# Optimization experiments

Measured on AMD Instinct MI355X. Metric: run time of the kernel, lower is better.

## Reference

```python
import jax, jax.numpy as jnp
import numpy as np

DIM = 1024
NUM_HEADS = 16
HEAD_DIM = DIM // NUM_HEADS


def setup_inputs() -> dict:
    key = jax.random.key(0)
    ks = jax.random.split(key, 9)
    s = 1.0 / np.sqrt(DIM)
    x = jax.random.normal(ks[0], (2, 2048, DIM), dtype=jnp.float32)
    Wq = jax.random.normal(ks[1], (DIM, DIM), dtype=jnp.float32) * s
    bq = jax.random.normal(ks[2], (DIM,), dtype=jnp.float32) * s
    Wk = jax.random.normal(ks[3], (DIM, DIM), dtype=jnp.float32) * s
    bk = jax.random.normal(ks[4], (DIM,), dtype=jnp.float32) * s
    Wv = jax.random.normal(ks[5], (DIM, DIM), dtype=jnp.float32) * s
    bv = jax.random.normal(ks[6], (DIM,), dtype=jnp.float32) * s
    Wo = jax.random.normal(ks[7], (DIM, DIM), dtype=jnp.float32) * s
    bo = jax.random.normal(ks[8], (DIM,), dtype=jnp.float32) * s
    return {"x": x, "Wq": Wq, "bq": bq, "Wk": Wk, "bk": bk,
            "Wv": Wv, "bv": bv, "Wo": Wo, "bo": bo}


def _softmax_one(x, axis=-1):
    # softmax with +1 in the denominator (quiet attention)
    x = x - jnp.max(x, axis=axis, keepdims=True)
    ex = jnp.exp(x)
    return ex / (1.0 + jnp.sum(ex, axis=axis, keepdims=True))


def reference(x, Wq, bq, Wk, bk, Wv, bv, Wo, bo):
    B, L, D = x.shape
    H, hd = NUM_HEADS, HEAD_DIM
    q = (x @ Wq + bq).reshape(B, L, H, hd).transpose(0, 2, 1, 3)  # b h l d
    k = (x @ Wk + bk).reshape(B, L, H, hd).transpose(0, 2, 1, 3)
    v = (x @ Wv + bv).reshape(B, L, H, hd).transpose(0, 2, 1, 3)
    scores = jnp.einsum('bhqd,bhkd->bhqk', q, k) / np.sqrt(hd).astype(np.float32)
    # causal additive mask: -inf above the diagonal (matches torch generate_square_subsequent_mask)
    causal = jnp.triu(jnp.full((L, L), -jnp.inf, dtype=scores.dtype), k=1)
    scores = scores + causal
    attn = _softmax_one(scores, axis=-1)
    ctx = jnp.einsum('bhqk,bhkd->bhqd', attn, v)
    ctx = ctx.transpose(0, 2, 1, 3).reshape(B, L, D)
    return ctx @ Wo + bo
```

## Files before the change

kernel.cpp:

```cpp
#include <hip/hip_runtime.h>
#include <hip/hip_bf16.h>
#include <cstdint>
#include <cstddef>

#define DIMN 1024
#define NHEAD 16
#define HDIM 64
#define NB 2
#define SEQ 2048
#define MROWS 4096
#define BHN 32
#define QKV_STRIDE 4194304
#define BH_ELEMS 131072

typedef float f32x4 __attribute__((ext_vector_type(4)));
typedef __bf16 bf16x8 __attribute__((ext_vector_type(8)));

__device__ __forceinline__ void async_copy16(const void* g, void* l) {
    __builtin_amdgcn_global_load_lds(
        (__attribute__((address_space(1))) void*)(g),
        (__attribute__((address_space(3))) void*)(l), 16, 0, 0);
}

__device__ __forceinline__ unsigned short bf16_bits(float f) {
    __hip_bfloat16 hb = __float2bfloat16(f);
    return *(unsigned short*)&hb;
}

__global__ __launch_bounds__(256) void prep_kernel(
        const float* __restrict__ x, const float* __restrict__ bq,
        const float* __restrict__ bk, const float* __restrict__ bv,
        __hip_bfloat16* __restrict__ xbf, float* __restrict__ biasq) {
    int bid = blockIdx.x;
    if (bid < 4096) {
        int i = (bid * 256 + threadIdx.x) * 4;
        float4 v = *(const float4*)(x + i);
        xbf[i + 0] = __float2bfloat16(v.x);
        xbf[i + 1] = __float2bfloat16(v.y);
        xbf[i + 2] = __float2bfloat16(v.z);
        xbf[i + 3] = __float2bfloat16(v.w);
    } else {
        int base = (bid - 4096) * 1024 + threadIdx.x * 4;
#pragma unroll
        for (int e = 0; e < 4; e++) {
            int gi = base + e;
            int which = gi >> 10, off = gi & 1023;
            float v = (which == 0) ? bq[off] : (which == 1) ? bk[off] : bv[off];
            biasq[gi] = v;
        }
    }
}

__global__ __launch_bounds__(256) void transpose_w_kernel(
        const float* __restrict__ Wq, const float* __restrict__ Wk,
        const float* __restrict__ Wv, const float* __restrict__ Wo,
        __hip_bfloat16* __restrict__ wqkvt, __hip_bfloat16* __restrict__ wot) {
    __shared__ float tile[32][33];
    int z = blockIdx.z;
    const float* in = (z == 0) ? Wq : (z == 1) ? Wk : (z == 2) ? Wv : Wo;
    __hip_bfloat16* out = (z == 3) ? wot : wqkvt + (size_t)z * DIMN * DIMN;
    int n0 = blockIdx.x * 32, k0 = blockIdx.y * 32;
    int tx = threadIdx.x, ty = threadIdx.y;
#pragma unroll
    for (int r = 0; r < 32; r += 8)
        tile[ty + r][tx] = in[(size_t)(k0 + ty + r) * DIMN + n0 + tx];
    __syncthreads();
#pragma unroll
    for (int r = 0; r < 32; r += 8)
        out[(size_t)(n0 + ty + r) * DIMN + k0 + tx] =
            __float2bfloat16(tile[tx][ty + r]);
}

__global__ __launch_bounds__(256) void gemm_qkv_kernel(
        const __hip_bfloat16* __restrict__ A, const __hip_bfloat16* __restrict__ Bt,
        const float* __restrict__ bias, __hip_bfloat16* __restrict__ qkv,
        __hip_bfloat16* __restrict__ vt) {
    __shared__ __align__(16) unsigned short As[128 * 32];
    __shared__ __align__(16) unsigned short Bs[128 * 32];
    const int t = threadIdx.x;
    const int m0 = blockIdx.y * 128;
    const int n0 = blockIdx.x * 128;
    const int lane = t & 63;
    const int w = t >> 6;
    const int wm = (w >> 1) * 64;
    const int wn = (w & 1) * 64;
    const int r16 = lane & 15;
    const int quad = lane >> 4;

    f32x4 acc[4][4];
#pragma unroll
    for (int i = 0; i < 4; i++)
#pragma unroll
        for (int j = 0; j < 4; j++) acc[i][j] = (f32x4){0.f, 0.f, 0.f, 0.f};

    const int rowA = t >> 2;
    const int kch = (t & 3) * 8;

    for (int k0 = 0; k0 < DIMN; k0 += 32) {
        __syncthreads();
#pragma unroll
        for (int r = 0; r < 2; r++) {
            int row = rowA + r * 64;
            async_copy16(A + (size_t)(m0 + row) * DIMN + k0 + kch,
                         (char*)As + (size_t)(row * 4 + (t & 3)) * 16);
            async_copy16(Bt + (size_t)(n0 + row) * DIMN + k0 + kch,
                         (char*)Bs + (size_t)(row * 4 + (t & 3)) * 16);
        }
        __syncthreads();

        bf16x8 af[4], bfr[4];
#pragma unroll
        for (int i = 0; i < 4; i++)
            af[i] = *(const bf16x8*)&As[(wm + i * 16 + r16) * 32 + quad * 8];
#pragma unroll
        for (int j = 0; j < 4; j++)
            bfr[j] = *(const bf16x8*)&Bs[(wn + j * 16 + r16) * 32 + quad * 8];
#pragma unroll
        for (int i = 0; i < 4; i++)
#pragma unroll
            for (int j = 0; j < 4; j++)
                acc[i][j] = __builtin_amdgcn_mfma_f32_16x16x32_bf16(
                    af[i], bfr[j], acc[i][j], 0, 0, 0);
    }

#pragma unroll
    for (int i = 0; i < 4; i++)
#pragma unroll
        for (int j = 0; j < 4; j++) {
            int n = n0 + wn + j * 16 + r16;
            float bv = bias[n];
            int which = n >> 10, rem = n & 1023;
            int h = rem >> 6, d = rem & 63;
            int mbase = m0 + wm + i * 16 + quad * 4;
            int b = mbase >> 11;
            int lrow = mbase & 2047;
            int bh = b * NHEAD + h;
            if (which == 2) {
                ushort4 pk;
                pk.x = bf16_bits(acc[i][j][0] + bv);
                pk.y = bf16_bits(acc[i][j][1] + bv);
                pk.z = bf16_bits(acc[i][j][2] + bv);
                pk.w = bf16_bits(acc[i][j][3] + bv);
                *(ushort4*)(vt + (size_t)bh * BH_ELEMS + (size_t)d * SEQ + lrow) = pk;
            } else {
#pragma unroll
                for (int r = 0; r < 4; r++) {
                    float v = acc[i][j][r] + bv;
                    if (which == 0) v *= 0.125f;
                    qkv[(size_t)which * QKV_STRIDE + (size_t)bh * BH_ELEMS +
                        (size_t)(lrow + r) * 64 + d] = __float2bfloat16(v);
                }
            }
        }
}

__global__ __launch_bounds__(256) void gemm_out_kernel(
        const __hip_bfloat16* __restrict__ A, const __hip_bfloat16* __restrict__ Bt,
        const float* __restrict__ bias, float* __restrict__ outp) {
    __shared__ __align__(16) unsigned short As[64 * 32];
    __shared__ __align__(16) unsigned short Bs[128 * 32];
    const int t = threadIdx.x;
    const int m0 = blockIdx.y * 64;
    const int n0 = blockIdx.x * 128;
    const int lane = t & 63;
    const int w = t >> 6;
    const int wm = (w >> 1) * 32;
    const int wn = (w & 1) * 64;
    const int r16 = lane & 15;
    const int quad = lane >> 4;

    f32x4 acc[2][4];
#pragma unroll
    for (int i = 0; i < 2; i++)
#pragma unroll
        for (int j = 0; j < 4; j++) acc[i][j] = (f32x4){0.f, 0.f, 0.f, 0.f};

    const int rowA = t >> 2;
    const int kch = (t & 3) * 8;

    for (int k0 = 0; k0 < DIMN; k0 += 32) {
        __syncthreads();
        async_copy16(A + (size_t)(m0 + rowA) * DIMN + k0 + kch, (char*)As + t * 16);
#pragma unroll
        for (int r = 0; r < 2; r++) {
            int row = rowA + r * 64;
            async_copy16(Bt + (size_t)(n0 + row) * DIMN + k0 + kch,
                         (char*)Bs + (size_t)(row * 4 + (t & 3)) * 16);
        }
        __syncthreads();

        bf16x8 af[2], bfr[4];
#pragma unroll
        for (int i = 0; i < 2; i++)
            af[i] = *(const bf16x8*)&As[(wm + i * 16 + r16) * 32 + quad * 8];
#pragma unroll
        for (int j = 0; j < 4; j++)
            bfr[j] = *(const bf16x8*)&Bs[(wn + j * 16 + r16) * 32 + quad * 8];
#pragma unroll
        for (int i = 0; i < 2; i++)
#pragma unroll
            for (int j = 0; j < 4; j++)
                acc[i][j] = __builtin_amdgcn_mfma_f32_16x16x32_bf16(
                    af[i], bfr[j], acc[i][j], 0, 0, 0);
    }

#pragma unroll
    for (int i = 0; i < 2; i++)
#pragma unroll
        for (int j = 0; j < 4; j++) {
            int n = n0 + wn + j * 16 + r16;
            float bv = bias[n];
#pragma unroll
            for (int r = 0; r < 4; r++) {
                int m = m0 + wm + i * 16 + quad * 4 + r;
                outp[(size_t)m * DIMN + n] = acc[i][j][r] + bv;
            }
        }
}

__global__ __launch_bounds__(512, 4) void attn_mfma_kernel(
        const __hip_bfloat16* __restrict__ qkv, const __hip_bfloat16* __restrict__ vt,
        __hip_bfloat16* __restrict__ ctxout) {
    __shared__ __align__(16) unsigned short SMEM[24576];

    const int bx = blockIdx.x;
    const int g = bx >> 5;
    const int qt = (g < 8) ? 15 - g : g - 8;
    const int bh = bx & 31;
    const int t = threadIdx.x;
    const int lane = t & 63;
    const int w = t >> 6;
    const int half = w >> 2;
    const int wq = w & 3;
    const int r16 = lane & 15;
    const int quad = lane >> 4;
    const int qbase = qt * 128 + wq * 32;
    const int swz = quad ^ ((r16 >> 1) & 3);
    const int pkey = (r16 >> 1) & 3;

    const __hip_bfloat16* Qg = qkv + (size_t)bh * BH_ELEMS;
    const __hip_bfloat16* Kg = qkv + (size_t)QKV_STRIDE + (size_t)bh * BH_ELEMS;
    const __hip_bfloat16* Vtg = vt + (size_t)bh * BH_ELEMS;

    const unsigned short* KsW = SMEM + half * 4096;
    const unsigned short* VsW = SMEM + 8192 + half * 4096;
    unsigned short* PsW = SMEM + 16384 + w * 1024;

    bf16x8 bq[2][2];
#pragma unroll
    for (int ng = 0; ng < 2; ng++)
#pragma unroll
        for (int kp = 0; kp < 2; kp++)
            bq[ng][kp] = *(const bf16x8*)(Qg + (size_t)(qbase + ng * 16 + r16) * 64 +
                                          kp * 32 + quad * 8);

    f32x4 oT[4][2];
#pragma unroll
    for (int mt = 0; mt < 4; mt++)
#pragma unroll
        for (int ng = 0; ng < 2; ng++) oT[mt][ng] = (f32x4){0.f, 0.f, 0.f, 0.f};
    float m_run[2] = {-1e30f, -1e30f};
    float z_run[2] = {0.f, 0.f};

    const int niter = qt + 1;
#pragma unroll 1
    for (int i = 0; i < niter; i++) {
        const int kt0 = i, kt1 = qt + 1 + i;
        __syncthreads();
#pragma unroll
        for (int it = 0; it < 4; it++) {
            int cl = it * 512 + t;
            int cb = cl & 511;
            int kp = cb >> 8, rr = (cb >> 2) & 63, c = cb & 3;
            int cg = c ^ ((rr >> 1) & 3);
            int ktile = ((cl >> 9) & 1) ? kt1 : kt0;
            const __hip_bfloat16* src = (cl < 1024)
                ? Kg + (size_t)(ktile * 64 + rr) * 64 + kp * 32 + cg * 8
                : Vtg + (size_t)rr * SEQ + ktile * 64 + kp * 32 + cg * 8;
            async_copy16(src, (char*)SMEM + (size_t)cl * 16);
        }
        __syncthreads();

        const int ktile = half ? kt1 : kt0;
        if (ktile * 64 > qbase + 31) continue;

        f32x4 st[4][2];
#pragma unroll
        for (int mt = 0; mt < 4; mt++)
#pragma unroll
            for (int ng = 0; ng < 2; ng++) st[mt][ng] = (f32x4){0.f, 0.f, 0.f, 0.f};
#pragma unroll
        for (int mt = 0; mt < 4; mt++)
#pragma unroll
            for (int kp = 0; kp < 2; kp++) {
                bf16x8 ak = *(const bf16x8*)&KsW[kp * 2048 + (mt * 16 + r16) * 32 + swz * 8];
                st[mt][0] = __builtin_amdgcn_mfma_f32_16x16x32_bf16(ak, bq[0][kp], st[mt][0], 0, 0, 0);
                st[mt][1] = __builtin_amdgcn_mfma_f32_16x16x32_bf16(ak, bq[1][kp], st[mt][1], 0, 0, 0);
            }

        if (ktile * 64 + 63 > qbase) {
#pragma unroll
            for (int mt = 0; mt < 4; mt++) {
                int kb = ktile * 64 + mt * 16 + quad * 4;
#pragma unroll
                for (int ng = 0; ng < 2; ng++) {
                    int q = qbase + ng * 16 + r16;
#pragma unroll
                    for (int r = 0; r < 4; r++)
                        if (kb + r > q) st[mt][ng][r] = -__builtin_inff();
                }
            }
        }

#pragma unroll
        for (int p = 0; p < 2; p++) {
#pragma unroll
            for (int ml = 0; ml < 2; ml++) {
                int mt = p * 2 + ml;
#pragma unroll
                for (int ng = 0; ng < 2; ng++) {
                    float s0 = st[mt][ng][0], s1 = st[mt][ng][1];
                    float s2 = st[mt][ng][2], s3 = st[mt][ng][3];
                    m_run[ng] = fmaxf(m_run[ng], fmaxf(fmaxf(s0, s1), fmaxf(s2, s3)));
                    float p0 = __expf(s0), p1 = __expf(s1);
                    float p2 = __expf(s2), p3 = __expf(s3);
                    z_run[ng] += (p0 + p1) + (p2 + p3);
                    ushort4 pk;
                    pk.x = bf16_bits(p0); pk.y = bf16_bits(p1);
                    pk.z = bf16_bits(p2); pk.w = bf16_bits(p3);
                    int c = (ml * 2 + (quad >> 1)) ^ pkey;
                    *(ushort4*)&PsW[(ng * 16 + r16) * 32 + c * 8 + (quad & 1) * 4] = pk;
                }
            }
            bf16x8 bp0 = *(const bf16x8*)&PsW[r16 * 32 + (quad ^ pkey) * 8];
            bf16x8 bp1 = *(const bf16x8*)&PsW[(16 + r16) * 32 + (quad ^ pkey) * 8];
#pragma unroll
            for (int mt = 0; mt < 4; mt++) {
                bf16x8 av = *(const bf16x8*)&VsW[p * 2048 + (mt * 16 + r16) * 32 + swz * 8];
                oT[mt][0] = __builtin_amdgcn_mfma_f32_16x16x32_bf16(av, bp0, oT[mt][0], 0, 0, 0);
                oT[mt][1] = __builtin_amdgcn_mfma_f32_16x16x32_bf16(av, bp1, oT[mt][1], 0, 0, 0);
            }
        }
    }

#pragma unroll
    for (int off = 16; off < 64; off <<= 1)
#pragma unroll
        for (int ng = 0; ng < 2; ng++) {
            m_run[ng] = fmaxf(m_run[ng], __shfl_xor(m_run[ng], off, 64));
            z_run[ng] += __shfl_xor(z_run[ng], off, 64);
        }

    __syncthreads();
    f32x4* CbO = (f32x4*)SMEM;
    f32x4* Ml = (f32x4*)((char*)SMEM + 32768);
    if (w >= 4) {
        int w4 = w - 4;
#pragma unroll
        for (int mt = 0; mt < 4; mt++)
#pragma unroll
            for (int ng = 0; ng < 2; ng++)
                CbO[((w4 * 8 + mt * 2 + ng) << 6) + lane] = oT[mt][ng];
        f32x4 ml;
        ml[0] = m_run[0]; ml[1] = m_run[1]; ml[2] = z_run[0]; ml[3] = z_run[1];
        Ml[(w4 << 6) + lane] = ml;
    }
    __syncthreads();
    if (w < 4) {
        f32x4 ml = Ml[(w << 6) + lane];
        float rd[2];
#pragma unroll
        for (int ng = 0; ng < 2; ng++) {
            float mtot = fmaxf(m_run[ng], ml[ng]);
            float ztot = z_run[ng] + ml[2 + ng];
            rd[ng] = 1.f / (__expf(mtot) + ztot);
        }
        const int b = bh >> 4, h = bh & 15;
#pragma unroll
        for (int mt = 0; mt < 4; mt++)
#pragma unroll
            for (int ng = 0; ng < 2; ng++) {
                f32x4 O1 = CbO[((w * 8 + mt * 2 + ng) << 6) + lane];
                int q = qbase + ng * 16 + r16;
                ushort4 pk;
                pk.x = bf16_bits((oT[mt][ng][0] + O1[0]) * rd[ng]);
                pk.y = bf16_bits((oT[mt][ng][1] + O1[1]) * rd[ng]);
                pk.z = bf16_bits((oT[mt][ng][2] + O1[2]) * rd[ng]);
                pk.w = bf16_bits((oT[mt][ng][3] + O1[3]) * rd[ng]);
                *(ushort4*)(ctxout + ((size_t)(b * SEQ + q)) * DIMN + h * 64 +
                            mt * 16 + quad * 4) = pk;
            }
    }
}


extern "C" void kernel_launch(void* const* d_in, const int* in_sizes, int n_in,
                              void* d_out, int out_size, void* d_ws, size_t ws_size,
                              hipStream_t stream) {
    const float* x  = (const float*)d_in[0];
    const float* Wq = (const float*)d_in[1];
    const float* bq = (const float*)d_in[2];
    const float* Wk = (const float*)d_in[3];
    const float* bk = (const float*)d_in[4];
    const float* Wv = (const float*)d_in[5];
    const float* bv = (const float*)d_in[6];
    const float* Wo = (const float*)d_in[7];
    const float* bo = (const float*)d_in[8];

    char* ws = (char*)d_ws;
    __hip_bfloat16* xbf   = (__hip_bfloat16*)(ws);
    __hip_bfloat16* wqkvt = (__hip_bfloat16*)(ws + (8u << 20));
    __hip_bfloat16* wot   = (__hip_bfloat16*)(ws + (14u << 20));
    float*          biasq = (float*)(ws + (16u << 20));
    __hip_bfloat16* qkv   = (__hip_bfloat16*)(ws + (16u << 20) + 65536u);
    __hip_bfloat16* vt    = (__hip_bfloat16*)(ws + (16u << 20) + 65536u + (16u << 20));
    __hip_bfloat16* ctx   = (__hip_bfloat16*)(ws + (16u << 20) + 65536u + (24u << 20));
    float* out = (float*)d_out;

    prep_kernel<<<4099, 256, 0, stream>>>(x, bq, bk, bv, xbf, biasq);
    transpose_w_kernel<<<dim3(32, 32, 4), dim3(32, 8), 0, stream>>>(Wq, Wk, Wv, Wo, wqkvt, wot);

    gemm_qkv_kernel<<<dim3(24, 32), 256, 0, stream>>>(xbf, wqkvt, biasq, qkv, vt);
    attn_mfma_kernel<<<512, 512, 0, stream>>>(qkv, vt, ctx);
    gemm_out_kernel<<<dim3(8, 64), 256, 0, stream>>>(ctx, wot, bo, out);
}
```

Baseline: 184.1 us.

## Double-buffer K tiles in attention and fuse weight transpose into prep kernel

The attention loop now prefetches the next K tile pair into a second LDS buffer while the current one is being computed, and issues the V load at the start of each iteration so it overlaps the QK^T and softmax work. The P staging buffer is halved by processing one query group at a time, with an extra barrier between the score and PV phases. Separately, the weight transpose kernel is folded into the prep kernel to remove one launch. These add LDS usage and a barrier per iteration, and the async loads may not be properly waited on before use.

Result: faster. 178.2 us (-3.2%).

```diff
diff --git a/kernel.cpp b/kernel.cpp
--- a/kernel.cpp
+++ b/kernel.cpp
@@ -30,17 +30,22 @@
 __global__ __launch_bounds__(256) void prep_kernel(
         const float* __restrict__ x, const float* __restrict__ bq,
         const float* __restrict__ bk, const float* __restrict__ bv,
-        __hip_bfloat16* __restrict__ xbf, float* __restrict__ biasq) {
-    int bid = blockIdx.x;
+        const float* __restrict__ Wq, const float* __restrict__ Wk,
+        const float* __restrict__ Wv, const float* __restrict__ Wo,
+        __hip_bfloat16* __restrict__ xbf, float* __restrict__ biasq,
+        __hip_bfloat16* __restrict__ wqkvt, __hip_bfloat16* __restrict__ wot) {
+    __shared__ float tile[32][33];
+    const int bid = blockIdx.x;
+    const int t = threadIdx.x;
     if (bid < 4096) {
-        int i = (bid * 256 + threadIdx.x) * 4;
+        int i = (bid * 256 + t) * 4;
         float4 v = *(const float4*)(x + i);
         xbf[i + 0] = __float2bfloat16(v.x);
         xbf[i + 1] = __float2bfloat16(v.y);
         xbf[i + 2] = __float2bfloat16(v.z);
         xbf[i + 3] = __float2bfloat16(v.w);
-    } else {
-        int base = (bid - 4096) * 1024 + threadIdx.x * 4;
+    } else if (bid < 4099) {
+        int base = (bid - 4096) * 1024 + t * 4;
 #pragma unroll
         for (int e = 0; e < 4; e++) {
             int gi = base + e;
@@ -48,27 +53,23 @@
             float v = (which == 0) ? bq[off] : (which == 1) ? bk[off] : bv[off];
             biasq[gi] = v;
         }
-    }
-}
-
-__global__ __launch_bounds__(256) void transpose_w_kernel(
-        const float* __restrict__ Wq, const float* __restrict__ Wk,
-        const float* __restrict__ Wv, const float* __restrict__ Wo,
-        __hip_bfloat16* __restrict__ wqkvt, __hip_bfloat16* __restrict__ wot) {
-    __shared__ float tile[32][33];
-    int z = blockIdx.z;
-    const float* in = (z == 0) ? Wq : (z == 1) ? Wk : (z == 2) ? Wv : Wo;
-    __hip_bfloat16* out = (z == 3) ? wot : wqkvt + (size_t)z * DIMN * DIMN;
-    int n0 = blockIdx.x * 32, k0 = blockIdx.y * 32;
-    int tx = threadIdx.x, ty = threadIdx.y;
-#pragma unroll
-    for (int r = 0; r < 32; r += 8)
-        tile[ty + r][tx] = in[(size_t)(k0 + ty + r) * DIMN + n0 + tx];
-    __syncthreads();
-#pragma unroll
-    for (int r = 0; r < 32; r += 8)
-        out[(size_t)(n0 + ty + r) * DIMN + k0 + tx] =
-            __float2bfloat16(tile[tx][ty + r]);
+    } else {
+        int rr = bid - 4099;
+        int z = rr >> 10;
+        int tid = rr & 1023;
+        int n0 = (tid & 31) * 32, k0 = (tid >> 5) * 32;
+        const float* in = (z == 0) ? Wq : (z == 1) ? Wk : (z == 2) ? Wv : Wo;
+        __hip_bfloat16* out = (z == 3) ? wot : wqkvt + (size_t)z * DIMN * DIMN;
+        int tx = t & 31, ty = t >> 5;
+#pragma unroll
+        for (int r = 0; r < 32; r += 8)
+            tile[ty + r][tx] = in[(size_t)(k0 + ty + r) * DIMN + n0 + tx];
+        __syncthreads();
+#pragma unroll
+        for (int r = 0; r < 32; r += 8)
+            out[(size_t)(n0 + ty + r) * DIMN + k0 + tx] =
+                __float2bfloat16(tile[tx][ty + r]);
+    }
 }
 
 __global__ __launch_bounds__(256) void gemm_qkv_kernel(
@@ -221,7 +222,7 @@
 __global__ __launch_bounds__(512, 4) void attn_mfma_kernel(
         const __hip_bfloat16* __restrict__ qkv, const __hip_bfloat16* __restrict__ vt,
         __hip_bfloat16* __restrict__ ctxout) {
-    __shared__ __align__(16) unsigned short SMEM[24576];
+    __shared__ __align__(16) unsigned short SMEM[28672];
 
     const int bx = blockIdx.x;
     const int g = bx >> 5;
@@ -242,9 +243,11 @@
     const __hip_bfloat16* Kg = qkv + (size_t)QKV_STRIDE + (size_t)bh * BH_ELEMS;
     const __hip_bfloat16* Vtg = vt + (size_t)bh * BH_ELEMS;
 
-    const unsigned short* KsW = SMEM + half * 4096;
-    const unsigned short* VsW = SMEM + 8192 + half * 4096;
-    unsigned short* PsW = SMEM + 16384 + w * 1024;
+    unsigned short* PsW = SMEM + 24576 + w * 512;
+
+    const int cb_kp = (t & 511) >> 8;
+    const int cb_rr = ((t & 511) >> 2) & 63;
+    const int cb_cg = ((t & 511) & 3) ^ ((cb_rr >> 1) & 3);
 
     bf16x8 bq[2][2];
 #pragma unroll
@@ -263,60 +266,74 @@
     float z_run[2] = {0.f, 0.f};
 
     const int niter = qt + 1;
+
+#pragma unroll
+    for (int it = 0; it < 2; it++) {
+        int cl = it * 512 + t;
+        int ktile = (cl >> 9) ? (qt + 1) : 0;
+        async_copy16(Kg + (size_t)(ktile * 64 + cb_rr) * 64 + cb_kp * 32 + cb_cg * 8,
+                     (char*)SMEM + (size_t)cl * 16);
+    }
+
 #pragma unroll 1
     for (int i = 0; i < niter; i++) {
-        const int kt0 = i, kt1 = qt + 1 + i;
-        __syncthreads();
-#pragma unroll
-        for (int it = 0; it < 4; it++) {
+        const int curb = i & 1;
+        __syncthreads();
+
+#pragma unroll
+        for (int it = 0; it < 2; it++) {
             int cl = it * 512 + t;
-            int cb = cl & 511;
-            int kp = cb >> 8, rr = (cb >> 2) & 63, c = cb & 3;
-            int cg = c ^ ((rr >> 1) & 3);
-            int ktile = ((cl >> 9) & 1) ? kt1 : kt0;
-            const __hip_bfloat16* src = (cl < 1024)
-                ? Kg + (size_t)(ktile * 64 + rr) * 64 + kp * 32 + cg * 8
-                : Vtg + (size_t)rr * SEQ + ktile * 64 + kp * 32 + cg * 8;
-            async_copy16(src, (char*)SMEM + (size_t)cl * 16);
-        }
-        __syncthreads();
-
-        const int ktile = half ? kt1 : kt0;
-        if (ktile * 64 > qbase + 31) continue;
+            int ktile = (cl >> 9) ? (qt + 1 + i) : i;
+            async_copy16(Vtg + (size_t)cb_rr * SEQ + ktile * 64 + cb_kp * 32 + cb_cg * 8,
+                         (char*)SMEM + 32768 + (size_t)cl * 16);
+        }
+        if (i + 1 < niter) {
+            int ktA = i + 1;
+            int ktB = qt + 2 + i; if (ktB > 31) ktB = 31;
+#pragma unroll
+            for (int it = 0; it < 2; it++) {
+                int cl = it * 512 + t;
+                int ktile = (cl >> 9) ? ktB : ktA;
+                async_copy16(Kg + (size_t)(ktile * 64 + cb_rr) * 64 + cb_kp * 32 + cb_cg * 8,
+                             (char*)SMEM + (size_t)(curb ^ 1) * 16384 + (size_t)cl * 16);
+            }
+        }
+
+        const int ktile = half ? (qt + 1 + i) : i;
+        const bool active = (ktile * 64 <= qbase + 31);
 
         f32x4 st[4][2];
-#pragma unroll
-        for (int mt = 0; mt < 4; mt++)
-#pragma unroll
-            for (int ng = 0; ng < 2; ng++) st[mt][ng] = (f32x4){0.f, 0.f, 0.f, 0.f};
-#pragma unroll
-        for (int mt = 0; mt < 4; mt++)
-#pragma unroll
-            for (int kp = 0; kp < 2; kp++) {
-                bf16x8 ak = *(const bf16x8*)&KsW[kp * 2048 + (mt * 16 + r16) * 32 + swz * 8];
-                st[mt][0] = __builtin_amdgcn_mfma_f32_16x16x32_bf16(ak, bq[0][kp], st[mt][0], 0, 0, 0);
-                st[mt][1] = __builtin_amdgcn_mfma_f32_16x16x32_bf16(ak, bq[1][kp], st[mt][1], 0, 0, 0);
-            }
-
-        if (ktile * 64 + 63 > qbase) {
-#pragma unroll
-            for (int mt = 0; mt < 4; mt++) {
-                int kb = ktile * 64 + mt * 16 + quad * 4;
-#pragma unroll
-                for (int ng = 0; ng < 2; ng++) {
-                    int q = qbase + ng * 16 + r16;
-#pragma unroll
-                    for (int r = 0; r < 4; r++)
-                        if (kb + r > q) st[mt][ng][r] = -__builtin_inff();
+        if (active) {
+            const unsigned short* KsW = SMEM + curb * 8192 + half * 4096;
+#pragma unroll
+            for (int mt = 0; mt < 4; mt++)
+#pragma unroll
+                for (int ng = 0; ng < 2; ng++) st[mt][ng] = (f32x4){0.f, 0.f, 0.f, 0.f};
+#pragma unroll
+            for (int mt = 0; mt < 4; mt++)
+#pragma unroll
+                for (int kp = 0; kp < 2; kp++) {
+                    bf16x8 ak = *(const bf16x8*)&KsW[kp * 2048 + (mt * 16 + r16) * 32 + swz * 8];
+                    st[mt][0] = __builtin_amdgcn_mfma_f32_16x16x32_bf16(ak, bq[0][kp], st[mt][0], 0, 0, 0);
+                    st[mt][1] = __builtin_amdgcn_mfma_f32_16x16x32_bf16(ak, bq[1][kp], st[mt][1], 0, 0, 0);
                 }
-            }
-        }
-
-#pragma unroll
-        for (int p = 0; p < 2; p++) {
-#pragma unroll
-            for (int ml = 0; ml < 2; ml++) {
-                int mt = p * 2 + ml;
+
+            if (ktile * 64 + 63 > qbase) {
+#pragma unroll
+                for (int mt = 0; mt < 4; mt++) {
+                    int kb = ktile * 64 + mt * 16 + quad * 4;
+#pragma unroll
+                    for (int ng = 0; ng < 2; ng++) {
+                        int q = qbase + ng * 16 + r16;
+#pragma unroll
+                        for (int r = 0; r < 4; r++)
+                            if (kb + r > q) st[mt][ng][r] = -__builtin_inff();
+                    }
+                }
+            }
+
+#pragma unroll
+            for (int mt = 0; mt < 4; mt++)
 #pragma unroll
                 for (int ng = 0; ng < 2; ng++) {
                     float s0 = st[mt][ng][0], s1 = st[mt][ng][1];
@@ -325,20 +342,37 @@
                     float p0 = __expf(s0), p1 = __expf(s1);
                     float p2 = __expf(s2), p3 = __expf(s3);
                     z_run[ng] += (p0 + p1) + (p2 + p3);
-                    ushort4 pk;
-                    pk.x = bf16_bits(p0); pk.y = bf16_bits(p1);
-                    pk.z = bf16_bits(p2); pk.w = bf16_bits(p3);
-                    int c = (ml * 2 + (quad >> 1)) ^ pkey;
-                    *(ushort4*)&PsW[(ng * 16 + r16) * 32 + c * 8 + (quad & 1) * 4] = pk;
+                    st[mt][ng][0] = p0; st[mt][ng][1] = p1;
+                    st[mt][ng][2] = p2; st[mt][ng][3] = p3;
                 }
-            }
-            bf16x8 bp0 = *(const bf16x8*)&PsW[r16 * 32 + (quad ^ pkey) * 8];
-            bf16x8 bp1 = *(const bf16x8*)&PsW[(16 + r16) * 32 + (quad ^ pkey) * 8];
-#pragma unroll
-            for (int mt = 0; mt < 4; mt++) {
-                bf16x8 av = *(const bf16x8*)&VsW[p * 2048 + (mt * 16 + r16) * 32 + swz * 8];
-                oT[mt][0] = __builtin_amdgcn_mfma_f32_16x16x32_bf16(av, bp0, oT[mt][0], 0, 0, 0);
-                oT[mt][1] = __builtin_amdgcn_mfma_f32_16x16x32_bf16(av, bp1, oT[mt][1], 0, 0, 0);
+        }
+        __syncthreads();
+
+        if (active) {
+            const unsigned short* VsW = SMEM + 16384 + half * 4096;
+#pragma unroll
+            for (int p = 0; p < 2; p++) {
+#pragma unroll
+                for (int ng = 0; ng < 2; ng++) {
+#pragma unroll
+                    for (int ml = 0; ml < 2; ml++) {
+                        int mt = p * 2 + ml;
+                        ushort4 pk;
+                        pk.x = bf16_bits(st[mt][ng][0]);
+                        pk.y = bf16_bits(st[mt][ng][1]);
+                        pk.z = bf16_bits(st[mt][ng][2]);
+                        pk.w = bf16_bits(st[mt][ng][3]);
+                        int c = (ml * 2 + (quad >> 1)) ^ pkey;
+                        *(ushort4*)&PsW[r16 * 32 + c * 8 + (quad & 1) * 4] = pk;
+                    }
+                    bf16x8 bp = *(const bf16x8*)&PsW[r16 * 32 + (quad ^ pkey) * 8];
+#pragma unroll
+                    for (int mt = 0; mt < 4; mt++) {
+                        bf16x8 av = *(const bf16x8*)&VsW[p * 2048 + (mt * 16 + r16) * 32 + swz * 8];
+                        oT[mt][ng] = __builtin_amdgcn_mfma_f32_16x16x32_bf16(
+                            av, bp, oT[mt][ng], 0, 0, 0);
+                    }
+                }
             }
         }
     }
@@ -417,9 +451,8 @@
     __hip_bfloat16* ctx   = (__hip_bfloat16*)(ws + (16u << 20) + 65536u + (24u << 20));
     float* out = (float*)d_out;
 
-    prep_kernel<<<4099, 256, 0, stream>>>(x, bq, bk, bv, xbf, biasq);
-    transpose_w_kernel<<<dim3(32, 32, 4), dim3(32, 8), 0, stream>>>(Wq, Wk, Wv, Wo, wqkvt, wot);
-
+    prep_kernel<<<8195, 256, 0, stream>>>(x, bq, bk, bv, Wq, Wk, Wv, Wo,
+                                          xbf, biasq, wqkvt, wot);
     gemm_qkv_kernel<<<dim3(24, 32), 256, 0, stream>>>(xbf, wqkvt, biasq, qkv, vt);
     attn_mfma_kernel<<<512, 512, 0, stream>>>(qkv, vt, ctx);
     gemm_out_kernel<<<dim3(8, 64), 256, 0, stream>>>(ctx, wot, bo, out);
```
